# Kernel optimization log

Hardware: AMD Instinct MI355X
Metric: run time of the kernel (lower is better)

The kernel has to match this reference:

```python
import jax, jax.numpy as jnp
import numpy as np

B, MQ, MK = 8, 512, 2048
Q_DIM, KV_DIM = 1024, 256
H = 8
QKC, VC = 1024, 1024
DQ, DV = QKC // H, VC // H
EPS = 1e-5  # nn.LayerNorm default


def _layer_norm(x, w, b):
    m = jnp.mean(x, axis=-1, keepdims=True)
    v = jnp.var(x, axis=-1, keepdims=True)
    return (x - m) * jax.lax.rsqrt(v + EPS) * w + b


def setup_inputs() -> dict:
    key = jax.random.key(0)
    ks = jax.random.split(key, 12)
    hidden_states = jax.random.normal(ks[0], (B, MQ, Q_DIM), dtype=jnp.float32)
    inputs = jax.random.normal(ks[1], (B, MK, KV_DIM), dtype=jnp.float32)
    # ragged per-batch kv lengths -> prefix-valid mask (matches keys[i, :n] packing)
    lengths = jax.random.randint(ks[2], (B,), MK // 4, MK + 1)
    inputs_mask = (jnp.arange(MK)[None, :] < lengths[:, None]).astype(jnp.int32)
    s = 0.02
    return {
        "hidden_states": hidden_states,
        "inputs": inputs,
        "inputs_mask": inputs_mask,
        "ln1_w": jnp.ones((Q_DIM,), jnp.float32),
        "ln1_b": jnp.zeros((Q_DIM,), jnp.float32),
        "ln2_w": jnp.ones((KV_DIM,), jnp.float32),
        "ln2_b": jnp.zeros((KV_DIM,), jnp.float32),
        "Wq": s * jax.random.normal(ks[3], (Q_DIM, QKC), dtype=jnp.float32),
        "bq": jnp.zeros((QKC,), jnp.float32),
        "Wk": s * jax.random.normal(ks[4], (KV_DIM, QKC), dtype=jnp.float32),
        "bk": jnp.zeros((QKC,), jnp.float32),
        "Wv": s * jax.random.normal(ks[5], (KV_DIM, VC), dtype=jnp.float32),
        "bv": jnp.zeros((VC,), jnp.float32),
    }


def reference(hidden_states, inputs, inputs_mask, ln1_w, ln1_b, ln2_w, ln2_b,
              Wq, bq, Wk, bk, Wv, bv):
    hs = _layer_norm(hidden_states, ln1_w, ln1_b)      # [B, MQ, Q_DIM]
    kv = _layer_norm(inputs, ln2_w, ln2_b)             # [B, MK, KV_DIM]

    q = (hs @ Wq + bq).reshape(B, MQ, H, DQ)           # [B, MQ, H, DQ]
    k = (kv @ Wk + bk).reshape(B, MK, H, DQ)           # [B, MK, H, DQ]
    v = (kv @ Wv + bv).reshape(B, MK, H, DV)           # [B, MK, H, DV]

    scores = jnp.einsum("bqhd,bkhd->bhqk", q, k) / jnp.sqrt(jnp.float32(DQ))
    mask_f = inputs_mask.astype(scores.dtype)          # [B, MK]
    neg = jnp.finfo(scores.dtype).min
    scores = scores + (1.0 - mask_f)[:, None, None, :] * neg
    probs = jax.nn.softmax(scores, axis=-1)            # [B, H, MQ, MK]

    ctx = jnp.einsum("bhqk,bkhd->bqhd", probs, v)      # [B, MQ, H, DV]
    return ctx.reshape(B, MQ, H * DV)
```

## Files before the change

### kernel.cpp

```cpp
#include <hip/hip_runtime.h>

#define DI __device__ __forceinline__

typedef _Float16 f16x8 __attribute__((ext_vector_type(8)));
typedef _Float16 f16x4 __attribute__((ext_vector_type(4)));
typedef float    f32x4 __attribute__((ext_vector_type(4)));

namespace {

constexpr int kB  = 8;
constexpr int kMQ = 512;
constexpr int kMK = 2048;
constexpr int kQKC = 1024;
constexpr int kVC  = 1024;

DI void gload16(const void* g, void* l) {
  __builtin_amdgcn_global_load_lds(
      (const __attribute__((address_space(1))) void*)g,
      (__attribute__((address_space(3))) void*)l, 16, 0, 0);
}

DI f32x4 mfma16(f16x8 a, f16x8 b, f32x4 c) {
  return __builtin_amdgcn_mfma_f32_16x16x32_f16(a, b, c, 0, 0, 0);
}

DI f32x4 mfma16k16(f16x4 a, f16x4 b, f32x4 c) {
  return __builtin_amdgcn_mfma_f32_16x16x16f16(a, b, c, 0, 0, 0);
}

template<int K, int N>
DI void transpose_dev(const float* __restrict__ W, _Float16* __restrict__ WT,
                      int bid, float (*t)[65]) {
  int nt = bid % (N / 64), kt = bid / (N / 64);
  int k0 = kt * 64, n0 = nt * 64;
  int tid = threadIdx.x;
#pragma unroll
  for (int j = 0; j < 16; ++j) {
    int e = tid + j * 256;
    int r = e >> 6, c = e & 63;
    t[r][c] = W[(size_t)(k0 + r) * N + n0 + c];
  }
  __syncthreads();
#pragma unroll
  for (int j = 0; j < 16; ++j) {
    int e = tid + j * 256;
    int r = e >> 6, c = e & 63;
    WT[(size_t)(n0 + r) * K + k0 + c] = (_Float16)t[c][r];
  }
}

DI void ln1024_dev(const float* __restrict__ x, const float* __restrict__ w,
                   const float* __restrict__ bb, _Float16* __restrict__ y,
                   int row, float* red) {
  int tid = threadIdx.x;
  const float4* xr = (const float4*)(x + (size_t)row * 1024);
  float4 v = xr[tid];
  float s = v.x + v.y + v.z + v.w;
  float q = v.x * v.x + v.y * v.y + v.z * v.z + v.w * v.w;
#pragma unroll
  for (int m = 32; m; m >>= 1) { s += __shfl_xor(s, m); q += __shfl_xor(q, m); }
  if ((tid & 63) == 0) { red[tid >> 6] = s; red[4 + (tid >> 6)] = q; }
  __syncthreads();
  s = red[0] + red[1] + red[2] + red[3];
  q = red[4] + red[5] + red[6] + red[7];
  float mean = s * (1.0f / 1024.0f);
  float var = q * (1.0f / 1024.0f) - mean * mean;
  float inv = rsqrtf(var + 1e-5f);
  f16x4 o;
  const float* wp = w + tid * 4;
  const float* bp = bb + tid * 4;
  o[0] = (_Float16)((v.x - mean) * inv * wp[0] + bp[0]);
  o[1] = (_Float16)((v.y - mean) * inv * wp[1] + bp[1]);
  o[2] = (_Float16)((v.z - mean) * inv * wp[2] + bp[2]);
  o[3] = (_Float16)((v.w - mean) * inv * wp[3] + bp[3]);
  *(f16x4*)(y + (size_t)row * 1024 + tid * 4) = o;
}

DI void ln256_dev(const float* __restrict__ x, const float* __restrict__ w,
                  const float* __restrict__ bb, _Float16* __restrict__ y, int bid) {
  int tid = threadIdx.x;
  int lane = tid & 63, wv = tid >> 6;
  size_t row = (size_t)bid * 4 + wv;
  const float4* xr = (const float4*)(x + row * 256);
  float4 v = xr[lane];
  float s = v.x + v.y + v.z + v.w;
  float q = v.x * v.x + v.y * v.y + v.z * v.z + v.w * v.w;
#pragma unroll
  for (int m = 32; m; m >>= 1) { s += __shfl_xor(s, m); q += __shfl_xor(q, m); }
  float mean = s * (1.0f / 256.0f);
  float var = q * (1.0f / 256.0f) - mean * mean;
  float inv = rsqrtf(var + 1e-5f);
  f16x4 o;
  const float* wp = w + lane * 4;
  const float* bp = bb + lane * 4;
  o[0] = (_Float16)((v.x - mean) * inv * wp[0] + bp[0]);
  o[1] = (_Float16)((v.y - mean) * inv * wp[1] + bp[1]);
  o[2] = (_Float16)((v.z - mean) * inv * wp[2] + bp[2]);
  o[3] = (_Float16)((v.w - mean) * inv * wp[3] + bp[3]);
  *(f16x4*)(y + row * 256 + lane * 4) = o;
}

__global__ __launch_bounds__(256) void prep_all(
    const float* __restrict__ Wq, const float* __restrict__ Wk, const float* __restrict__ Wv,
    _Float16* __restrict__ WqT, _Float16* __restrict__ WkT, _Float16* __restrict__ WvT,
    const float* __restrict__ hs, const float* __restrict__ ln1w, const float* __restrict__ ln1b,
    _Float16* __restrict__ hsln,
    const float* __restrict__ xin, const float* __restrict__ ln2w, const float* __restrict__ ln2b,
    _Float16* __restrict__ kvln) {
  __shared__ float tbuf[64][65];
  int bid = blockIdx.x;
  if (bid < 256) {
    transpose_dev<1024, 1024>(Wq, WqT, bid, tbuf);
  } else if (bid < 320) {
    transpose_dev<256, 1024>(Wk, WkT, bid - 256, tbuf);
  } else if (bid < 384) {
    transpose_dev<256, 1024>(Wv, WvT, bid - 320, tbuf);
  } else if (bid < 4480) {
    ln1024_dev(hs, ln1w, ln1b, hsln, bid - 384, (float*)tbuf);
  } else {
    ln256_dev(xin, ln2w, ln2b, kvln, bid - 4480);
  }
}

template<int M, int N, int K, bool BIAS_ROW, int MMODE, bool CM>
DI void gemm_dev(const _Float16* __restrict__ A, const _Float16* __restrict__ Bt,
                 const float* __restrict__ bias, const int* __restrict__ msk,
                 _Float16* __restrict__ C, int bid,
                 _Float16 (*As)[128 * 64], _Float16 (*Bs)[128 * 64]) {
  int tid = threadIdx.x, lane = tid & 63;
  int w = tid >> 6, wr = w >> 1, wc = w & 1;
  constexpr int NT = N / 128;
  constexpr int MT = M / 128;
  constexpr int KT = K / 64;
  int mt, nt;
  if constexpr (CM) { mt = bid % MT; nt = bid / MT; }
  else              { mt = bid / NT; nt = bid % NT; }
  if constexpr (MMODE == 1) { if (msk[mt * 128] == 0) return; }
  if constexpr (MMODE == 2) { if (msk[nt * 128] == 0) return; }
  const int l15 = lane & 15, l4 = lane >> 4;

  f32x4 acc[4][4] = {};

  const int rS = tid >> 3;
  const int cpS = tid & 7;

  auto stage = [&](int kt, int bufi) {
#pragma unroll
    for (int j = 0; j < 4; ++j) {
      int rr = rS + j * 32;
      int cg = cpS ^ (rr & 7);
      gload16(A  + ((size_t)(mt * 128 + rr) * K + kt * 64 + cg * 8),
              (char*)As[bufi] + j * 4096 + tid * 16);
      gload16(Bt + ((size_t)(nt * 128 + rr) * K + kt * 64 + cg * 8),
              (char*)Bs[bufi] + j * 4096 + tid * 16);
    }
  };

  stage(0, 0);
  __syncthreads();

  for (int kt = 0; kt < KT; ++kt) {
    int cur = kt & 1;
    if (kt + 1 < KT) stage(kt + 1, cur ^ 1);
#pragma unroll
    for (int ss = 0; ss < 2; ++ss) {
      f16x8 a[4], b[4];
#pragma unroll
      for (int m = 0; m < 4; ++m) {
        int ra = wr * 64 + m * 16 + l15;
        int cl = ss * 4 + l4;
        a[m] = *(const f16x8*)((const char*)As[cur] + ra * 128 + ((cl ^ (ra & 7)) << 4));
        int rb = wc * 64 + m * 16 + l15;
        b[m] = *(const f16x8*)((const char*)Bs[cur] + rb * 128 + ((cl ^ (rb & 7)) << 4));
      }
#pragma unroll
      for (int m = 0; m < 4; ++m)
#pragma unroll
        for (int n = 0; n < 4; ++n)
          acc[m][n] = mfma16(a[m], b[n], acc[m][n]);
    }
    __syncthreads();
  }

#pragma unroll
  for (int m = 0; m < 4; ++m) {
#pragma unroll
    for (int n = 0; n < 4; ++n) {
      int gi0 = mt * 128 + wr * 64 + m * 16 + l4 * 4;
      int gj  = nt * 128 + wc * 64 + n * 16 + l15;
#pragma unroll
      for (int r = 0; r < 4; ++r) {
        int gi = gi0 + r;
        float v = acc[m][n][r] + (BIAS_ROW ? bias[gi] : bias[gj]);
        C[(size_t)gi * N + gj] = (_Float16)v;
      }
    }
  }
}

__global__ __launch_bounds__(256) void gemm_all(
    const _Float16* __restrict__ hsln, const _Float16* __restrict__ WqT,
    const float* __restrict__ bq, _Float16* __restrict__ qbf,
    const _Float16* __restrict__ kvln, const _Float16* __restrict__ WkT,
    const float* __restrict__ bk, _Float16* __restrict__ kbf,
    const _Float16* __restrict__ WvT, const float* __restrict__ bv,
    _Float16* __restrict__ vT, const int* __restrict__ msk) {
  __shared__ _Float16 As[2][128 * 64];
  __shared__ _Float16 Bs[2][128 * 64];
  int bid = blockIdx.x;
  if (bid < 256) {
    gemm_dev<4096, 1024, 1024, false, 0, true>(hsln, WqT, bq, nullptr, qbf, bid, As, Bs);
  } else if (bid < 1280) {
    gemm_dev<16384, 1024, 256, false, 1, true>(kvln, WkT, bk, msk, kbf, bid - 256, As, Bs);
  } else {
    gemm_dev<1024, 16384, 256, true, 2, false>(WvT, kvln, bv, msk, vT, bid - 1280, As, Bs);
  }
}

__global__ __launch_bounds__(256, 2) void attn_kernel(const _Float16* __restrict__ qm,
                                                      const _Float16* __restrict__ km,
                                                      const _Float16* __restrict__ vT,
                                                      const int* __restrict__ msk,
                                                      float* __restrict__ out) {
  __shared__ _Float16 Ks[2][64 * 128];
  __shared__ _Float16 Vst[2][128 * 64];

  int tid = threadIdx.x, lane = tid & 63, w = tid >> 6;
  int bh = blockIdx.x & 63, qt = blockIdx.x >> 6;
  int h = bh & 7, b = bh >> 3;
  const int l15 = lane & 15, l4 = lane >> 4;

  int vld = (lane < 32) ? msk[b * kMK + lane * 64] : 0;
  int ntiles = __popcll(__ballot(vld != 0));
  int lv = msk[b * kMK + (ntiles - 1) * 64 + lane];
  int lastlen = __popcll(__ballot(lv != 0));

  f16x8 qf[4];
#pragma unroll
  for (int kc = 0; kc < 4; ++kc)
    qf[kc] = *(const f16x8*)(qm +
        (size_t)(b * kMQ + qt * 64 + w * 16 + l15) * kQKC +
        h * 128 + kc * 32 + l4 * 8);

  f32x4 o[8] = {};
  float rm = -1e30f, rl = 0.0f;

  const float sl2 = 0.08838834764831845f * 1.4426950408889634f;

  const int rK = tid >> 4, cpK = tid & 15;
  const int rV = tid >> 3, cpV = tid & 7;

  auto stage = [&](int kt, int bufi) {
#pragma unroll
    for (int j = 0; j < 4; ++j) {
      int rr = rK + j * 16;
      int cg = cpK ^ (rr & 7);
      gload16(km + (size_t)(b * kMK + kt * 64 + rr) * kQKC + h * 128 + cg * 8,
              (char*)Ks[bufi] + j * 4096 + tid * 16);
    }
#pragma unroll
    for (int j = 0; j < 4; ++j) {
      int dv = rV + j * 32;
      int cg = cpV ^ (dv & 7);
      gload16(vT + (size_t)(h * 128 + dv) * (kB * kMK) + (size_t)b * kMK + kt * 64 + cg * 8,
              (char*)Vst[bufi] + j * 4096 + tid * 16);
    }
  };

  stage(0, 0);
  __syncthreads();

  for (int kt = 0; kt < ntiles; ++kt) {
    int cur = kt & 1;
    if (kt + 1 < ntiles) stage(kt + 1, cur ^ 1);

    f32x4 sc[4] = {};
    __builtin_amdgcn_s_setprio(1);
#pragma unroll
    for (int kc = 0; kc < 4; ++kc) {
      f16x8 kb[4];
#pragma unroll
      for (int kf = 0; kf < 4; ++kf) {
        int rr = kf * 16 + l15;
        int cl = kc * 4 + l4;
        kb[kf] = *(const f16x8*)((const char*)Ks[cur] + rr * 256 + ((cl ^ (rr & 7)) << 4));
      }
#pragma unroll
      for (int kf = 0; kf < 4; ++kf)
        sc[kf] = mfma16(kb[kf], qf[kc], sc[kf]);
    }
    __builtin_amdgcn_s_setprio(0);

    if (kt == ntiles - 1) {
#pragma unroll
      for (int kf = 0; kf < 4; ++kf)
#pragma unroll
        for (int r = 0; r < 4; ++r)
          if (kf * 16 + l4 * 4 + r >= lastlen) sc[kf][r] = -3e38f;
    }

    float mx = sc[0][0];
#pragma unroll
    for (int kf = 0; kf < 4; ++kf)
#pragma unroll
      for (int r = 0; r < 4; ++r) mx = fmaxf(mx, sc[kf][r]);
    mx = fmaxf(mx, __shfl_xor(mx, 16));
    mx = fmaxf(mx, __shfl_xor(mx, 32));
    float al = 1.0f;
    if (__any(mx > rm)) {
      float nm = fmaxf(rm, mx);
      al = __builtin_amdgcn_exp2f((rm - nm) * sl2);
      rm = nm;
#pragma unroll
      for (int n = 0; n < 8; ++n)
#pragma unroll
        for (int r = 0; r < 4; ++r) o[n][r] *= al;
    }
    float nms = rm * sl2;
    float ts = 0.0f;
#pragma unroll
    for (int kf = 0; kf < 4; ++kf)
#pragma unroll
      for (int r = 0; r < 4; ++r) {
        float p = __builtin_amdgcn_exp2f(sc[kf][r] * sl2 - nms);
        sc[kf][r] = p;
        ts += p;
      }
    ts += __shfl_xor(ts, 16);
    ts += __shfl_xor(ts, 32);
    rl = rl * al + ts;

    f16x4 pb[4];
#pragma unroll
    for (int kf = 0; kf < 4; ++kf)
#pragma unroll
      for (int r = 0; r < 4; ++r) pb[kf][r] = (_Float16)sc[kf][r];

    __builtin_amdgcn_s_setprio(1);
#pragma unroll
    for (int n = 0; n < 8; ++n) {
      int dv = n * 16 + l15;
#pragma unroll
      for (int kf = 0; kf < 4; ++kf) {
        int phys = (kf * 2 + (l4 >> 1)) ^ (l15 & 7);
        f16x4 vb = *(const f16x4*)((const char*)Vst[cur] +
                                   dv * 128 + (phys << 4) + (l4 & 1) * 8);
        o[n] = mfma16k16(vb, pb[kf], o[n]);
      }
    }
    __builtin_amdgcn_s_setprio(0);
    __syncthreads();
  }

  float inv = 1.0f / rl;
  int qg = qt * 64 + w * 16 + l15;
#pragma unroll
  for (int n = 0; n < 8; ++n) {
    f32x4 ov;
#pragma unroll
    for (int r = 0; r < 4; ++r) ov[r] = o[n][r] * inv;
    *(f32x4*)(out + ((size_t)b * kMQ + qg) * kVC + h * 128 + n * 16 + l4 * 4) = ov;
  }
}

}

extern "C" void kernel_launch(void* const* d_in, const int* in_sizes, int n_in,
                              void* d_out, int out_size, void* d_ws, size_t ws_size,
                              hipStream_t stream) {
  (void)in_sizes; (void)n_in; (void)out_size; (void)ws_size;
  const float* hs   = (const float*)d_in[0];
  const float* xin  = (const float*)d_in[1];
  const int*   msk  = (const int*)d_in[2];
  const float* ln1w = (const float*)d_in[3];
  const float* ln1b = (const float*)d_in[4];
  const float* ln2w = (const float*)d_in[5];
  const float* ln2b = (const float*)d_in[6];
  const float* Wq   = (const float*)d_in[7];
  const float* bq   = (const float*)d_in[8];
  const float* Wk   = (const float*)d_in[9];
  const float* bk   = (const float*)d_in[10];
  const float* Wv   = (const float*)d_in[11];
  const float* bv   = (const float*)d_in[12];
  float* out = (float*)d_out;

  char* ws = (char*)d_ws;
  _Float16* qbf  = (_Float16*)(ws + 0);
  _Float16* kbf  = (_Float16*)(ws + 8388608);
  _Float16* vT   = (_Float16*)(ws + 41943040);
  _Float16* hsln = (_Float16*)(ws + 75497472);
  _Float16* kvln = (_Float16*)(ws + 83886080);
  _Float16* WqT  = (_Float16*)(ws + 92274688);
  _Float16* WkT  = (_Float16*)(ws + 94371840);
  _Float16* WvT  = (_Float16*)(ws + 94896128);

  prep_all<<<8576, 256, 0, stream>>>(Wq, Wk, Wv, WqT, WkT, WvT,
                                     hs, ln1w, ln1b, hsln,
                                     xin, ln2w, ln2b, kvln);
  gemm_all<<<2304, 256, 0, stream>>>(hsln, WqT, bq, qbf,
                                     kvln, WkT, bk, kbf,
                                     WvT, bv, vT, msk);
  attn_kernel<<<512, 256, 0, stream>>>(qbf, kbf, vT, msk, out);
}
```

Baseline: 117.5 us.

## Split each attention KV tile across two wave groups and merge softmax states

The attention block grows from 256 to 512 threads. Two groups of four waves each handle half of every 64-key tile for the same 16 query rows, and each group keeps its own running max, sum and output accumulator. At the end the second group writes its partial output and softmax statistics to shared memory (reusing the K buffer), and the first group combines them with rescaling before storing. This doubles the waves working on each tile and halves per-wave MFMA work, to get more latency hiding on a grid of only 512 blocks. The cost is an extra merge pass through LDS, duplicated Q fragment loads, and launch bounds that force tighter register limits.

```diff
diff --git a/kernel.cpp b/kernel.cpp
--- a/kernel.cpp
+++ b/kernel.cpp
@@ -217,18 +217,21 @@
   }
 }
 
-__global__ __launch_bounds__(256, 2) void attn_kernel(const _Float16* __restrict__ qm,
+__global__ __launch_bounds__(512, 4) void attn_kernel(const _Float16* __restrict__ qm,
                                                       const _Float16* __restrict__ km,
                                                       const _Float16* __restrict__ vT,
                                                       const int* __restrict__ msk,
                                                       float* __restrict__ out) {
   __shared__ _Float16 Ks[2][64 * 128];
   __shared__ _Float16 Vst[2][128 * 64];
+  __shared__ float mlbuf[64][2];
 
   int tid = threadIdx.x, lane = tid & 63, w = tid >> 6;
   int bh = blockIdx.x & 63, qt = blockIdx.x >> 6;
   int h = bh & 7, b = bh >> 3;
   const int l15 = lane & 15, l4 = lane >> 4;
+  const int wq = w & 3;
+  const int g  = w >> 2;
 
   int vld = (lane < 32) ? msk[b * kMK + lane * 64] : 0;
   int ntiles = __popcll(__ballot(vld != 0));
@@ -239,7 +242,7 @@
 #pragma unroll
   for (int kc = 0; kc < 4; ++kc)
     qf[kc] = *(const f16x8*)(qm +
-        (size_t)(b * kMQ + qt * 64 + w * 16 + l15) * kQKC +
+        (size_t)(b * kMQ + qt * 64 + wq * 16 + l15) * kQKC +
         h * 128 + kc * 32 + l4 * 8);
 
   f32x4 o[8] = {};
@@ -252,18 +255,18 @@
 
   auto stage = [&](int kt, int bufi) {
 #pragma unroll
-    for (int j = 0; j < 4; ++j) {
-      int rr = rK + j * 16;
+    for (int j = 0; j < 2; ++j) {
+      int rr = rK + j * 32;
       int cg = cpK ^ (rr & 7);
       gload16(km + (size_t)(b * kMK + kt * 64 + rr) * kQKC + h * 128 + cg * 8,
-              (char*)Ks[bufi] + j * 4096 + tid * 16);
-    }
-#pragma unroll
-    for (int j = 0; j < 4; ++j) {
-      int dv = rV + j * 32;
+              (char*)Ks[bufi] + j * 8192 + tid * 16);
+    }
+#pragma unroll
+    for (int j = 0; j < 2; ++j) {
+      int dv = rV + j * 64;
       int cg = cpV ^ (dv & 7);
       gload16(vT + (size_t)(h * 128 + dv) * (kB * kMK) + (size_t)b * kMK + kt * 64 + cg * 8,
-              (char*)Vst[bufi] + j * 4096 + tid * 16);
+              (char*)Vst[bufi] + j * 8192 + tid * 16);
     }
   };
 
@@ -274,34 +277,34 @@
     int cur = kt & 1;
     if (kt + 1 < ntiles) stage(kt + 1, cur ^ 1);
 
-    f32x4 sc[4] = {};
+    f32x4 sc[2] = {};
     __builtin_amdgcn_s_setprio(1);
 #pragma unroll
     for (int kc = 0; kc < 4; ++kc) {
-      f16x8 kb[4];
-#pragma unroll
-      for (int kf = 0; kf < 4; ++kf) {
-        int rr = kf * 16 + l15;
+      f16x8 kb[2];
+#pragma unroll
+      for (int kf = 0; kf < 2; ++kf) {
+        int rr = g * 32 + kf * 16 + l15;
         int cl = kc * 4 + l4;
         kb[kf] = *(const f16x8*)((const char*)Ks[cur] + rr * 256 + ((cl ^ (rr & 7)) << 4));
       }
 #pragma unroll
-      for (int kf = 0; kf < 4; ++kf)
+      for (int kf = 0; kf < 2; ++kf)
         sc[kf] = mfma16(kb[kf], qf[kc], sc[kf]);
     }
     __builtin_amdgcn_s_setprio(0);
 
     if (kt == ntiles - 1) {
 #pragma unroll
-      for (int kf = 0; kf < 4; ++kf)
+      for (int kf = 0; kf < 2; ++kf)
 #pragma unroll
         for (int r = 0; r < 4; ++r)
-          if (kf * 16 + l4 * 4 + r >= lastlen) sc[kf][r] = -3e38f;
+          if (g * 32 + kf * 16 + l4 * 4 + r >= lastlen) sc[kf][r] = -3e38f;
     }
 
     float mx = sc[0][0];
 #pragma unroll
-    for (int kf = 0; kf < 4; ++kf)
+    for (int kf = 0; kf < 2; ++kf)
 #pragma unroll
       for (int r = 0; r < 4; ++r) mx = fmaxf(mx, sc[kf][r]);
     mx = fmaxf(mx, __shfl_xor(mx, 16));
@@ -319,7 +322,7 @@
     float nms = rm * sl2;
     float ts = 0.0f;
 #pragma unroll
-    for (int kf = 0; kf < 4; ++kf)
+    for (int kf = 0; kf < 2; ++kf)
 #pragma unroll
       for (int r = 0; r < 4; ++r) {
         float p = __builtin_amdgcn_exp2f(sc[kf][r] * sl2 - nms);
@@ -330,9 +333,9 @@
     ts += __shfl_xor(ts, 32);
     rl = rl * al + ts;
 
-    f16x4 pb[4];
-#pragma unroll
-    for (int kf = 0; kf < 4; ++kf)
+    f16x4 pb[2];
+#pragma unroll
+    for (int kf = 0; kf < 2; ++kf)
 #pragma unroll
       for (int r = 0; r < 4; ++r) pb[kf][r] = (_Float16)sc[kf][r];
 
@@ -341,8 +344,8 @@
     for (int n = 0; n < 8; ++n) {
       int dv = n * 16 + l15;
 #pragma unroll
-      for (int kf = 0; kf < 4; ++kf) {
-        int phys = (kf * 2 + (l4 >> 1)) ^ (l15 & 7);
+      for (int kf = 0; kf < 2; ++kf) {
+        int phys = (g * 4 + kf * 2 + (l4 >> 1)) ^ (dv & 7);
         f16x4 vb = *(const f16x4*)((const char*)Vst[cur] +
                                    dv * 128 + (phys << 4) + (l4 & 1) * 8);
         o[n] = mfma16k16(vb, pb[kf], o[n]);
@@ -352,13 +355,38 @@
     __syncthreads();
   }
 
-  float inv = 1.0f / rl;
-  int qg = qt * 64 + w * 16 + l15;
+  float* Mbuf = (float*)Ks;
+  if (g == 1) {
+#pragma unroll
+    for (int n = 0; n < 8; ++n)
+#pragma unroll
+      for (int r = 0; r < 4; ++r)
+        Mbuf[(n * 16 + l4 * 4 + r) * 64 + wq * 16 + l15] = o[n][r];
+    if (l4 == 0) {
+      mlbuf[wq * 16 + l15][0] = rm;
+      mlbuf[wq * 16 + l15][1] = rl;
+    }
+  }
+  __syncthreads();
+  if (g == 1) return;
+
+  float m1 = mlbuf[wq * 16 + l15][0];
+  float l1 = mlbuf[wq * 16 + l15][1];
+  float m = fmaxf(rm, m1);
+  float w0 = __builtin_amdgcn_exp2f((rm - m) * sl2);
+  float w1 = __builtin_amdgcn_exp2f((m1 - m) * sl2);
+  float inv = 1.0f / (rl * w0 + l1 * w1);
+  w0 *= inv; w1 *= inv;
+
+  int qg = qt * 64 + wq * 16 + l15;
 #pragma unroll
   for (int n = 0; n < 8; ++n) {
     f32x4 ov;
 #pragma unroll
-    for (int r = 0; r < 4; ++r) ov[r] = o[n][r] * inv;
+    for (int r = 0; r < 4; ++r) {
+      float o1 = Mbuf[(n * 16 + l4 * 4 + r) * 64 + wq * 16 + l15];
+      ov[r] = o[n][r] * w0 + o1 * w1;
+    }
     *(f32x4*)(out + ((size_t)b * kMQ + qg) * kVC + h * 128 + n * 16 + l4 * 4) = ov;
   }
 }
@@ -400,5 +428,5 @@
   gemm_all<<<2304, 256, 0, stream>>>(hsln, WqT, bq, qbf,
                                      kvln, WkT, bk, kbf,
                                      WvT, bv, vT, msk);
-  attn_kernel<<<512, 256, 0, stream>>>(qbf, kbf, vT, msk, out);
-}
+  attn_kernel<<<512, 512, 0, stream>>>(qbf, kbf, vT, msk, out);
+}
```

Measured after the change: 122.0 us. 1.04x slower.
